# Kernel optimization log

Hardware: AMD Instinct MI355X
Metric: run time of the kernel (lower is better)

Reference implementation:

```python
import jax, jax.numpy as jnp
import numpy as np

N = 100000
E = 3200000
IN_DIM, HID_DIM, OUT_DIM = 29, 64, 2


def setup_inputs() -> dict:
    key = jax.random.key(0)
    k1, k2, k3, k4, k5 = jax.random.split(key, 5)
    x = jax.random.normal(k1, (N, IN_DIM), dtype=jnp.float32)
    edge_index = jax.random.randint(k2, (2, E), 0, N, dtype=jnp.int64)
    # GCNConv params: glorot-ish weights, zero bias (bias added after aggregation)
    W1 = jax.random.normal(k3, (IN_DIM, HID_DIM), dtype=jnp.float32) * (1.0 / np.sqrt(IN_DIM))
    b1 = jnp.zeros((HID_DIM,), dtype=jnp.float32)
    W2 = jax.random.normal(k4, (HID_DIM, OUT_DIM), dtype=jnp.float32) * (1.0 / np.sqrt(HID_DIM))
    b2 = jnp.zeros((OUT_DIM,), dtype=jnp.float32)
    return {"x": x, "edge_index": edge_index, "W1": W1, "b1": b1, "W2": W2, "b2": b2}


def _gcn_norm(edge_index, n_nodes):
    # PyG gcn_norm with add_self_loops=True, symmetric D^-1/2 A D^-1/2
    loop = jnp.arange(n_nodes, dtype=edge_index.dtype)
    src = jnp.concatenate([edge_index[0], loop])
    dst = jnp.concatenate([edge_index[1], loop])
    deg = jax.ops.segment_sum(jnp.ones_like(dst, dtype=jnp.float32), dst, num_segments=n_nodes)
    dinv = jnp.where(deg > 0, jax.lax.rsqrt(deg), 0.0)
    norm = dinv[src] * dinv[dst]  # [E + N]
    return src, dst, norm


def _gcn_conv(x, src, dst, norm, W, b):
    h = x @ W                      # [N, d_out] -- transform first (smaller msgs)
    msg = h[src] * norm[:, None]   # [E+N, d_out] gather + scale
    out = jax.ops.segment_sum(msg, dst, num_segments=x.shape[0])  # scatter-add
    return out + b


def reference(x, edge_index, W1, b1, W2, b2):
    src, dst, norm = _gcn_norm(edge_index, x.shape[0])
    h = _gcn_conv(x, src, dst, norm, W1, b1)
    h = jax.nn.relu(h)
    out = _gcn_conv(h, src, dst, norm, W2, b2)
    return out
```

## Files before the change

### kernel.cpp

```cpp
#include <hip/hip_runtime.h>

#define N_NODES 100000
#define N_EDGES 3200000
#define IN_DIM  29
#define HID_DIM 64
#define NBUCK   391
#define BNODES  256
#define CAP     10496
#define PEPT    16
#define PEPB    16384
#define PSTAGE  22272

#define OFF_CUR   0
#define OFF_ROWS  512
#define OFF_ROWE  100512
#define OFF_DINV  200512
#define OFF_ZS    300512
#define OFF_EBUF  500544
#define OFF_XS    4604480

static __device__ __forceinline__ unsigned short f2bf(float f) {
    unsigned u = __float_as_uint(f);
    u += 0x7fffu + ((u >> 16) & 1u);
    return (unsigned short)(u >> 16);
}

static __device__ __forceinline__ void unpack_add(float4& acc, uint2 a) {
    acc.x += __uint_as_float(a.x << 16);
    acc.y += __uint_as_float(a.x & 0xFFFF0000u);
    acc.z += __uint_as_float(a.y << 16);
    acc.w += __uint_as_float(a.y & 0xFFFF0000u);
}

__global__ __launch_bounds__(1024) void partition_kernel(const int* __restrict__ ei,
        int* __restrict__ gcursor, int* __restrict__ ebuf) {
    __shared__ int lhist[NBUCK];
    __shared__ int lcur[NBUCK];
    __shared__ int gbase[NBUCK];
    __shared__ int soff[NBUCK];
    __shared__ int sc[NBUCK];
    __shared__ int stage[PSTAGE];
    int tid = threadIdx.x;
    for (int i = tid; i < NBUCK; i += 1024) lhist[i] = 0;
    __syncthreads();

    int base = blockIdx.x * PEPB + tid * PEPT;
    bool valid = (base < N_EDGES);
    if (valid) {
        const int4* dp = (const int4*)(ei + N_EDGES + base);
        #pragma unroll
        for (int q = 0; q < 4; ++q) {
            int4 t = dp[q];
            atomicAdd(&lhist[t.x >> 8], 1); atomicAdd(&lhist[t.y >> 8], 1);
            atomicAdd(&lhist[t.z >> 8], 1); atomicAdd(&lhist[t.w >> 8], 1);
        }
    }
    __syncthreads();
    int c = 0, p = 0;
    if (tid < NBUCK) { c = lhist[tid]; p = (c + 15) & ~15; sc[tid] = p; }
    __syncthreads();
    for (int off = 1; off < NBUCK; off <<= 1) {
        int t = 0;
        if (tid < NBUCK && tid >= off) t = sc[tid - off];
        __syncthreads();
        if (tid < NBUCK) sc[tid] += t;
        __syncthreads();
    }
    if (tid < NBUCK) {
        int so = sc[tid] - p;
        soff[tid] = so;
        lcur[tid] = so;
        gbase[tid] = p ? (tid * CAP + atomicAdd(&gcursor[tid], p)) : 0;
    }
    __syncthreads();
    if (valid) {
        const int4* dp = (const int4*)(ei + N_EDGES + base);
        const int4* sp = (const int4*)(ei + base);
        #pragma unroll
        for (int q = 0; q < 4; ++q) {
            int4 d = dp[q];
            int4 s = sp[q];
            int pos;
            pos = atomicAdd(&lcur[d.x >> 8], 1); stage[pos] = s.x | ((d.x & 255) << 17);
            pos = atomicAdd(&lcur[d.y >> 8], 1); stage[pos] = s.y | ((d.y & 255) << 17);
            pos = atomicAdd(&lcur[d.z >> 8], 1); stage[pos] = s.z | ((d.z & 255) << 17);
            pos = atomicAdd(&lcur[d.w >> 8], 1); stage[pos] = s.w | ((d.w & 255) << 17);
        }
    }
    __syncthreads();
    if (tid < NBUCK) {
        int endReal = lcur[tid];
        int endPad  = soff[tid] + (((lhist[tid]) + 15) & ~15);
        for (int k = endReal; k < endPad; ++k) stage[k] = -1;
    }
    __syncthreads();
    int wv = tid >> 6, ln = tid & 63;
    for (int b = wv; b < NBUCK; b += 16) {
        int np = (lhist[b] + 15) & ~15;
        int so = soff[b], gb = gbase[b];
        for (int k = ln; k < np; k += 64)
            ebuf[gb + k] = stage[so + k];
    }
}

__global__ __launch_bounds__(1024) void bucketsort_kernel(const int* __restrict__ gcursor,
        int* __restrict__ ebuf, int* __restrict__ rowStart, int* __restrict__ rowEnd,
        float* __restrict__ dinv, const float* __restrict__ x,
        unsigned int* __restrict__ xsb, float* __restrict__ zs) {
    __shared__ int   cnt[BNODES];
    __shared__ int   cur[BNODES];
    __shared__ float dls[BNODES];
    __shared__ int   stage[CAP];
    __shared__ int   szp_sh;
    int b = blockIdx.x, tid = threadIdx.x;
    if (tid < BNODES) cnt[tid] = 0;
    __syncthreads();
    int base = b * CAP;
    int size = gcursor[b];

    for (int j = tid; j < size; j += 1024) {
        unsigned p = (unsigned)ebuf[base + j];
        if (p != 0xFFFFFFFFu) atomicAdd(&cnt[p >> 17], 1);
    }
    __syncthreads();

    int v = 0, vp = 0;
    if (tid < BNODES) { v = cnt[tid]; vp = (v + 7) & ~7; cur[tid] = vp; }
    __syncthreads();
    for (int off = 1; off < BNODES; off <<= 1) {
        int t = 0;
        if (tid < BNODES && tid >= off) t = cur[tid - off];
        __syncthreads();
        if (tid < BNODES) cur[tid] += t;
        __syncthreads();
    }
    if (tid < BNODES) {
        int excl = cur[tid] - vp;
        int node = b * BNODES + tid;
        if (node < N_NODES) {
            rowStart[node] = base + excl;
            rowEnd[node]   = base + excl + vp;
            float dn = rsqrtf((float)v + 1.0f);
            dinv[node] = dn;
            dls[tid] = dn;
        }
        if (tid == BNODES - 1) szp_sh = cur[tid];
        cur[tid] = excl;
        for (int p2 = excl + v; p2 < excl + vp; ++p2)
            stage[p2] = N_NODES;
    }
    __syncthreads();

    for (int j = tid; j < size; j += 1024) {
        unsigned p = (unsigned)ebuf[base + j];
        if (p != 0xFFFFFFFFu) {
            int pos = atomicAdd(&cur[p >> 17], 1);
            stage[pos] = p & 0x1FFFF;
        }
    }
    __syncthreads();
    int szp = szp_sh;
    for (int j = tid; j < szp; j += 1024)
        ebuf[base + j] = stage[j];

    for (int i = tid; i < BNODES * 16; i += 1024) {
        int dl = i >> 4, kp = i & 15;
        int nd = b * BNODES + dl;
        if (nd < N_NODES) {
            float dn = dls[dl];
            int k0 = kp * 2, k1 = k0 + 1;
            float f0 = (k0 < IN_DIM) ? x[nd * IN_DIM + k0] * dn : 0.0f;
            float f1 = (k1 < IN_DIM) ? x[nd * IN_DIM + k1] * dn : 0.0f;
            xsb[(size_t)nd * 16 + kp] = (unsigned)f2bf(f0) | ((unsigned)f2bf(f1) << 16);
        } else if (nd == N_NODES) {
            xsb[(size_t)nd * 16 + kp] = 0u;
        }
    }
    if (b == 0 && tid == 0) {
        zs[2 * N_NODES]     = 0.0f;
        zs[2 * N_NODES + 1] = 0.0f;
    }
}

#define XROW(i) (((unsigned)(i) << 6) | moff)

#define PREP(P, rs, re, node)                                            \
    int P##i0, P##i1, P##i2, P##i3, P##i4, P##i5;                        \
    {                                                                    \
        int relim = max((re) - 1, (rs));                                 \
        int j0 = (rs) + q;                                               \
        int t0 = ebuf[min(j0,      relim)];                              \
        int t1 = ebuf[min(j0 + 8,  relim)];                              \
        int t2 = ebuf[min(j0 + 16, relim)];                              \
        int t3 = ebuf[min(j0 + 24, relim)];                              \
        int t4 = ebuf[min(j0 + 32, relim)];                              \
        P##i0 = (j0      < (re)) ? t0 : N_NODES;                         \
        P##i1 = (j0 + 8  < (re)) ? t1 : N_NODES;                         \
        P##i2 = (j0 + 16 < (re)) ? t2 : N_NODES;                         \
        P##i3 = (j0 + 24 < (re)) ? t3 : N_NODES;                         \
        P##i4 = (j0 + 32 < (re)) ? t4 : N_NODES;                         \
        P##i5 = (q == 0) ? (node) : N_NODES;    \
    }

#define GATH(G, P)                                                       \
    uint2 G##0 = *(const uint2*)(xb + XROW(P##i0));                      \
    uint2 G##1 = *(const uint2*)(xb + XROW(P##i1));                      \
    uint2 G##2 = *(const uint2*)(xb + XROW(P##i2));                      \
    uint2 G##3 = *(const uint2*)(xb + XROW(P##i3));                      \
    uint2 G##4 = *(const uint2*)(xb + XROW(P##i4));                      \
    uint2 G##5 = *(const uint2*)(xb + XROW(P##i5));

#define UNP(acc, G)                                                      \
    unpack_add(acc, G##0); unpack_add(acc, G##1); unpack_add(acc, G##2); \
    unpack_add(acc, G##3); unpack_add(acc, G##4); unpack_add(acc, G##5);

#define TAIL(acc, rs, re)                                                \
    {                                                                    \
        int j = (rs) + q + 40;                                           \
        while (j < (re)) {                  \
            int s = ebuf[j];                                             \
            uint2 a = *(const uint2*)(xb + XROW(s));                     \
            unpack_add(acc, a);                                          \
            j += 8;                                                      \
        }                                                                \
    }

static __device__ __forceinline__ void mlp_store(float4 acc, int node, int lane,
        const float* w1s, const float* b1s, const float* w2s,
        const float* __restrict__ dinv, float* __restrict__ zs) {
    #pragma unroll
    for (int msk = 8; msk <= 32; msk <<= 1) {
        acc.x += __shfl_xor(acc.x, msk);
        acc.y += __shfl_xor(acc.y, msk);
        acc.z += __shfl_xor(acc.z, msk);
        acc.w += __shfl_xor(acc.w, msk);
    }
    float dn = dinv[node];
    acc.x *= dn; acc.y *= dn; acc.z *= dn; acc.w *= dn;

    float h = b1s[lane];
    #pragma unroll
    for (int kk = 0; kk < IN_DIM; ++kk) {
        float comp = ((kk & 3) == 0) ? acc.x : ((kk & 3) == 1) ? acc.y
                   : ((kk & 3) == 2) ? acc.z : acc.w;
        h = fmaf(__shfl(comp, kk >> 2), w1s[kk * HID_DIM + lane], h);
    }
    h = fmaxf(h, 0.0f);

    float z0 = h * w2s[lane * 2 + 0];
    float z1 = h * w2s[lane * 2 + 1];
    #pragma unroll
    for (int off = 32; off > 0; off >>= 1) {
        z0 += __shfl_down(z0, off);
        z1 += __shfl_down(z1, off);
    }
    if (lane == 0) {
        float2 o; o.x = z0 * dn; o.y = z1 * dn;
        *(float2*)(zs + node * 2) = o;
    }
}

__global__ __launch_bounds__(256) void fused_kernel(const unsigned int* __restrict__ xs_,
        const int* __restrict__ rowStart, const int* __restrict__ rowEnd,
        const int* __restrict__ ebuf, const float* __restrict__ dinv,
        const float* __restrict__ W1, const float* __restrict__ b1,
        const float* __restrict__ W2, float* __restrict__ zs) {
    __shared__ float w1s[IN_DIM * HID_DIM];
    __shared__ float b1s[HID_DIM];
    __shared__ float w2s[HID_DIM * 2];
    const int tid = threadIdx.x;
    for (int i = tid; i < IN_DIM * HID_DIM; i += 256) w1s[i] = W1[i];
    if (tid < HID_DIM) {
        b1s[tid] = b1[tid];
        w2s[tid * 2 + 0] = W2[tid * 2 + 0];
        w2s[tid * 2 + 1] = W2[tid * 2 + 1];
    }
    __syncthreads();

    const int lane = tid & 63;
    const int q = lane >> 3, m = lane & 7;
    const unsigned moff = (unsigned)(m << 3);
    const char* xb = (const char*)xs_;
    const int n0 = blockIdx.x * 16 + (tid >> 6) * 4;

    const int rs0 = rowStart[n0+0], re0 = rowEnd[n0+0];
    const int rs1 = rowStart[n0+1], re1 = rowEnd[n0+1];
    const int rs2 = rowStart[n0+2], re2 = rowEnd[n0+2];
    const int rs3 = rowStart[n0+3], re3 = rowEnd[n0+3];

    PREP(pa, rs0, re0, n0+0)
    GATH(ga, pa)
    PREP(pb, rs1, re1, n0+1)
    float4 acc0 = make_float4(0.f, 0.f, 0.f, 0.f);
    UNP(acc0, ga)
    TAIL(acc0, rs0, re0)
    GATH(gb, pb)
    PREP(pc, rs2, re2, n0+2)
    mlp_store(acc0, n0+0, lane, w1s, b1s, w2s, dinv, zs);

    float4 acc1 = make_float4(0.f, 0.f, 0.f, 0.f);
    UNP(acc1, gb)
    TAIL(acc1, rs1, re1)
    GATH(gc, pc)
    PREP(pd, rs3, re3, n0+3)
    mlp_store(acc1, n0+1, lane, w1s, b1s, w2s, dinv, zs);

    float4 acc2 = make_float4(0.f, 0.f, 0.f, 0.f);
    UNP(acc2, gc)
    TAIL(acc2, rs2, re2)
    GATH(gd, pd)
    mlp_store(acc2, n0+2, lane, w1s, b1s, w2s, dinv, zs);

    float4 acc3 = make_float4(0.f, 0.f, 0.f, 0.f);
    UNP(acc3, gd)
    TAIL(acc3, rs3, re3)
    mlp_store(acc3, n0+3, lane, w1s, b1s, w2s, dinv, zs);
}

__global__ __launch_bounds__(256) void agg2_kernel(const float* __restrict__ zs,
        const int* __restrict__ rowStart, const int* __restrict__ rowEnd,
        const int* __restrict__ ebuf, const float* __restrict__ dinv,
        const float* __restrict__ b2, float* __restrict__ out) {
    int tid = threadIdx.x;
    int node = blockIdx.x * 16 + (tid >> 4);
    if (node >= N_NODES) return;
    int gl = tid & 15;
    const float2* zs2 = (const float2*)zs;
    float a0 = 0.0f, a1 = 0.0f, c0 = 0.0f, c1 = 0.0f;
    int rs = rowStart[node], re = rowEnd[node];
    int j = rs + gl;
    for (; j + 16 < re; j += 32) {
        float2 za = zs2[ebuf[j]];
        float2 zb = zs2[ebuf[j + 16]];
        a0 += za.x; a1 += za.y;
        c0 += zb.x; c1 += zb.y;
    }
    if (j < re) {
        float2 za = zs2[ebuf[j]];
        a0 += za.x; a1 += za.y;
    }
    a0 += c0; a1 += c1;
    a0 += __shfl_xor(a0, 8); a1 += __shfl_xor(a1, 8);
    a0 += __shfl_xor(a0, 4); a1 += __shfl_xor(a1, 4);
    a0 += __shfl_xor(a0, 2); a1 += __shfl_xor(a1, 2);
    a0 += __shfl_xor(a0, 1); a1 += __shfl_xor(a1, 1);
    if (gl == 0) {
        float dn = dinv[node];
        float2 zself = zs2[node];
        float2 o;
        o.x = dn * (a0 + zself.x) + b2[0];
        o.y = dn * (a1 + zself.y) + b2[1];
        ((float2*)out)[node] = o;
    }
}

extern "C" void kernel_launch(void* const* d_in, const int* in_sizes, int n_in,
                              void* d_out, int out_size, void* d_ws, size_t ws_size,
                              hipStream_t stream) {
    const float* x  = (const float*)d_in[0];
    const int*   ei = (const int*)d_in[1];
    const float* W1 = (const float*)d_in[2];
    const float* b1 = (const float*)d_in[3];
    const float* W2 = (const float*)d_in[4];
    const float* b2 = (const float*)d_in[5];
    float* out = (float*)d_out;

    int*   wsi      = (int*)d_ws;
    float* wsf      = (float*)d_ws;
    int*   gcursor  = wsi + OFF_CUR;
    int*   rowStart = wsi + OFF_ROWS;
    int*   rowEnd   = wsi + OFF_ROWE;
    float* dinv     = wsf + OFF_DINV;
    float* zs       = wsf + OFF_ZS;
    int*   ebuf     = wsi + OFF_EBUF;
    unsigned int* xsb = (unsigned int*)(wsi + OFF_XS);

    hipMemsetAsync(gcursor, 0, NBUCK * sizeof(int), stream);
    partition_kernel<<<(N_EDGES + PEPB - 1) / PEPB, 1024, 0, stream>>>(ei, gcursor, ebuf);
    bucketsort_kernel<<<NBUCK, 1024, 0, stream>>>(gcursor, ebuf, rowStart, rowEnd, dinv, x, xsb, zs);
    fused_kernel<<<N_NODES / 16, 256, 0, stream>>>(xsb, rowStart, rowEnd, ebuf, dinv, W1, b1, W2, zs);
    agg2_kernel<<<(N_NODES + 15) / 16, 256, 0, stream>>>(zs, rowStart, rowEnd, ebuf, dinv, b2, out);
}
```

Before: 203.0 us.

## Split bf16 feature prep into its own kernel and pair MLP epilogues

Moves the scaled bf16 conversion of x out of bucketsort into a separate elementwise xs_kernel. Bucketsort now caches the raw partition entries in LDS and scatters sorted indices straight to global ebuf, dropping the LDS staging copy-back. The fused kernel moves to 512-thread blocks, issues more gathers earlier, and runs the MLP epilogue on two nodes at once so shuffles and FMAs can interleave. The cost is an extra kernel launch and scattered, uncoalesced global writes during the sort.

```diff
diff --git a/kernel.cpp b/kernel.cpp
--- a/kernel.cpp
+++ b/kernel.cpp
@@ -105,13 +105,10 @@
 
 __global__ __launch_bounds__(1024) void bucketsort_kernel(const int* __restrict__ gcursor,
         int* __restrict__ ebuf, int* __restrict__ rowStart, int* __restrict__ rowEnd,
-        float* __restrict__ dinv, const float* __restrict__ x,
-        unsigned int* __restrict__ xsb, float* __restrict__ zs) {
-    __shared__ int   cnt[BNODES];
-    __shared__ int   cur[BNODES];
-    __shared__ float dls[BNODES];
-    __shared__ int   stage[CAP];
-    __shared__ int   szp_sh;
+        float* __restrict__ dinv, float* __restrict__ zs) {
+    __shared__ int cnt[BNODES];
+    __shared__ int cur[BNODES];
+    __shared__ int stage[CAP];
     int b = blockIdx.x, tid = threadIdx.x;
     if (tid < BNODES) cnt[tid] = 0;
     __syncthreads();
@@ -120,6 +117,7 @@
 
     for (int j = tid; j < size; j += 1024) {
         unsigned p = (unsigned)ebuf[base + j];
+        stage[j] = (int)p;
         if (p != 0xFFFFFFFFu) atomicAdd(&cnt[p >> 17], 1);
     }
     __syncthreads();
@@ -140,46 +138,40 @@
         if (node < N_NODES) {
             rowStart[node] = base + excl;
             rowEnd[node]   = base + excl + vp;
-            float dn = rsqrtf((float)v + 1.0f);
-            dinv[node] = dn;
-            dls[tid] = dn;
+            dinv[node]     = rsqrtf((float)v + 1.0f);
+            for (int p2 = excl + v; p2 < excl + vp; ++p2)
+                ebuf[base + p2] = N_NODES;
         }
-        if (tid == BNODES - 1) szp_sh = cur[tid];
         cur[tid] = excl;
-        for (int p2 = excl + v; p2 < excl + vp; ++p2)
-            stage[p2] = N_NODES;
-    }
-    __syncthreads();
-
+    }
+    __syncthreads();
     for (int j = tid; j < size; j += 1024) {
-        unsigned p = (unsigned)ebuf[base + j];
+        unsigned p = (unsigned)stage[j];
         if (p != 0xFFFFFFFFu) {
             int pos = atomicAdd(&cur[p >> 17], 1);
-            stage[pos] = p & 0x1FFFF;
-        }
-    }
-    __syncthreads();
-    int szp = szp_sh;
-    for (int j = tid; j < szp; j += 1024)
-        ebuf[base + j] = stage[j];
-
-    for (int i = tid; i < BNODES * 16; i += 1024) {
-        int dl = i >> 4, kp = i & 15;
-        int nd = b * BNODES + dl;
-        if (nd < N_NODES) {
-            float dn = dls[dl];
-            int k0 = kp * 2, k1 = k0 + 1;
-            float f0 = (k0 < IN_DIM) ? x[nd * IN_DIM + k0] * dn : 0.0f;
-            float f1 = (k1 < IN_DIM) ? x[nd * IN_DIM + k1] * dn : 0.0f;
-            xsb[(size_t)nd * 16 + kp] = (unsigned)f2bf(f0) | ((unsigned)f2bf(f1) << 16);
-        } else if (nd == N_NODES) {
-            xsb[(size_t)nd * 16 + kp] = 0u;
+            ebuf[base + pos] = (int)(p & 0x1FFFF);
         }
     }
     if (b == 0 && tid == 0) {
         zs[2 * N_NODES]     = 0.0f;
         zs[2 * N_NODES + 1] = 0.0f;
     }
+}
+
+__global__ __launch_bounds__(256) void xs_kernel(const float* __restrict__ x,
+        const float* __restrict__ dinv, unsigned int* __restrict__ xsb) {
+    int i = blockIdx.x * 256 + threadIdx.x;
+    if (i >= (N_NODES + 1) * 16) return;
+    int nd = i >> 4, kp = i & 15;
+    unsigned u = 0u;
+    if (nd < N_NODES) {
+        float dn = dinv[nd];
+        int k0 = kp * 2, k1 = k0 + 1;
+        float f0 = (k0 < IN_DIM) ? x[nd * IN_DIM + k0] * dn : 0.0f;
+        float f1 = (k1 < IN_DIM) ? x[nd * IN_DIM + k1] * dn : 0.0f;
+        u = (unsigned)f2bf(f0) | ((unsigned)f2bf(f1) << 16);
+    }
+    xsb[i] = u;
 }
 
 #define XROW(i) (((unsigned)(i) << 6) | moff)
@@ -225,42 +217,50 @@
         }                                                                \
     }
 
-static __device__ __forceinline__ void mlp_store(float4 acc, int node, int lane,
+static __device__ __forceinline__ void mlp2_store(float4 aA, float4 aB,
+        int nodeA, int nodeB, int lane,
         const float* w1s, const float* b1s, const float* w2s,
         const float* __restrict__ dinv, float* __restrict__ zs) {
     #pragma unroll
     for (int msk = 8; msk <= 32; msk <<= 1) {
-        acc.x += __shfl_xor(acc.x, msk);
-        acc.y += __shfl_xor(acc.y, msk);
-        acc.z += __shfl_xor(acc.z, msk);
-        acc.w += __shfl_xor(acc.w, msk);
-    }
-    float dn = dinv[node];
-    acc.x *= dn; acc.y *= dn; acc.z *= dn; acc.w *= dn;
-
-    float h = b1s[lane];
+        aA.x += __shfl_xor(aA.x, msk); aB.x += __shfl_xor(aB.x, msk);
+        aA.y += __shfl_xor(aA.y, msk); aB.y += __shfl_xor(aB.y, msk);
+        aA.z += __shfl_xor(aA.z, msk); aB.z += __shfl_xor(aB.z, msk);
+        aA.w += __shfl_xor(aA.w, msk); aB.w += __shfl_xor(aB.w, msk);
+    }
+    float dnA = dinv[nodeA], dnB = dinv[nodeB];
+    aA.x *= dnA; aA.y *= dnA; aA.z *= dnA; aA.w *= dnA;
+    aB.x *= dnB; aB.y *= dnB; aB.z *= dnB; aB.w *= dnB;
+
+    float hA = b1s[lane], hB = b1s[lane];
     #pragma unroll
     for (int kk = 0; kk < IN_DIM; ++kk) {
-        float comp = ((kk & 3) == 0) ? acc.x : ((kk & 3) == 1) ? acc.y
-                   : ((kk & 3) == 2) ? acc.z : acc.w;
-        h = fmaf(__shfl(comp, kk >> 2), w1s[kk * HID_DIM + lane], h);
-    }
-    h = fmaxf(h, 0.0f);
-
-    float z0 = h * w2s[lane * 2 + 0];
-    float z1 = h * w2s[lane * 2 + 1];
+        float w = w1s[kk * HID_DIM + lane];
+        float cA = ((kk & 3) == 0) ? aA.x : ((kk & 3) == 1) ? aA.y
+                 : ((kk & 3) == 2) ? aA.z : aA.w;
+        float cB = ((kk & 3) == 0) ? aB.x : ((kk & 3) == 1) ? aB.y
+                 : ((kk & 3) == 2) ? aB.z : aB.w;
+        hA = fmaf(__shfl(cA, kk >> 2), w, hA);
+        hB = fmaf(__shfl(cB, kk >> 2), w, hB);
+    }
+    hA = fmaxf(hA, 0.0f); hB = fmaxf(hB, 0.0f);
+
+    float zA0 = hA * w2s[lane * 2 + 0], zA1 = hA * w2s[lane * 2 + 1];
+    float zB0 = hB * w2s[lane * 2 + 0], zB1 = hB * w2s[lane * 2 + 1];
     #pragma unroll
     for (int off = 32; off > 0; off >>= 1) {
-        z0 += __shfl_down(z0, off);
-        z1 += __shfl_down(z1, off);
+        zA0 += __shfl_down(zA0, off); zA1 += __shfl_down(zA1, off);
+        zB0 += __shfl_down(zB0, off); zB1 += __shfl_down(zB1, off);
     }
     if (lane == 0) {
-        float2 o; o.x = z0 * dn; o.y = z1 * dn;
-        *(float2*)(zs + node * 2) = o;
-    }
-}
-
-__global__ __launch_bounds__(256) void fused_kernel(const unsigned int* __restrict__ xs_,
+        float2 oA; oA.x = zA0 * dnA; oA.y = zA1 * dnA;
+        float2 oB; oB.x = zB0 * dnB; oB.y = zB1 * dnB;
+        *(float2*)(zs + nodeA * 2) = oA;
+        *(float2*)(zs + nodeB * 2) = oB;
+    }
+}
+
+__global__ __launch_bounds__(512) void fused_kernel(const unsigned int* __restrict__ xs_,
         const int* __restrict__ rowStart, const int* __restrict__ rowEnd,
         const int* __restrict__ ebuf, const float* __restrict__ dinv,
         const float* __restrict__ W1, const float* __restrict__ b1,
@@ -269,7 +269,7 @@
     __shared__ float b1s[HID_DIM];
     __shared__ float w2s[HID_DIM * 2];
     const int tid = threadIdx.x;
-    for (int i = tid; i < IN_DIM * HID_DIM; i += 256) w1s[i] = W1[i];
+    for (int i = tid; i < IN_DIM * HID_DIM; i += 512) w1s[i] = W1[i];
     if (tid < HID_DIM) {
         b1s[tid] = b1[tid];
         w2s[tid * 2 + 0] = W2[tid * 2 + 0];
@@ -281,7 +281,7 @@
     const int q = lane >> 3, m = lane & 7;
     const unsigned moff = (unsigned)(m << 3);
     const char* xb = (const char*)xs_;
-    const int n0 = blockIdx.x * 16 + (tid >> 6) * 4;
+    const int n0 = blockIdx.x * 32 + (tid >> 6) * 4;
 
     const int rs0 = rowStart[n0+0], re0 = rowEnd[n0+0];
     const int rs1 = rowStart[n0+1], re1 = rowEnd[n0+1];
@@ -289,32 +289,28 @@
     const int rs3 = rowStart[n0+3], re3 = rowEnd[n0+3];
 
     PREP(pa, rs0, re0, n0+0)
+    PREP(pb, rs1, re1, n0+1)
     GATH(ga, pa)
-    PREP(pb, rs1, re1, n0+1)
+    GATH(gb, pb)
+    PREP(pc, rs2, re2, n0+2)
+    PREP(pd, rs3, re3, n0+3)
     float4 acc0 = make_float4(0.f, 0.f, 0.f, 0.f);
+    float4 acc1 = make_float4(0.f, 0.f, 0.f, 0.f);
     UNP(acc0, ga)
     TAIL(acc0, rs0, re0)
-    GATH(gb, pb)
-    PREP(pc, rs2, re2, n0+2)
-    mlp_store(acc0, n0+0, lane, w1s, b1s, w2s, dinv, zs);
-
-    float4 acc1 = make_float4(0.f, 0.f, 0.f, 0.f);
     UNP(acc1, gb)
     TAIL(acc1, rs1, re1)
     GATH(gc, pc)
-    PREP(pd, rs3, re3, n0+3)
-    mlp_store(acc1, n0+1, lane, w1s, b1s, w2s, dinv, zs);
+    GATH(gd, pd)
+    mlp2_store(acc0, acc1, n0+0, n0+1, lane, w1s, b1s, w2s, dinv, zs);
 
     float4 acc2 = make_float4(0.f, 0.f, 0.f, 0.f);
+    float4 acc3 = make_float4(0.f, 0.f, 0.f, 0.f);
     UNP(acc2, gc)
     TAIL(acc2, rs2, re2)
-    GATH(gd, pd)
-    mlp_store(acc2, n0+2, lane, w1s, b1s, w2s, dinv, zs);
-
-    float4 acc3 = make_float4(0.f, 0.f, 0.f, 0.f);
     UNP(acc3, gd)
     TAIL(acc3, rs3, re3)
-    mlp_store(acc3, n0+3, lane, w1s, b1s, w2s, dinv, zs);
+    mlp2_store(acc2, acc3, n0+2, n0+3, lane, w1s, b1s, w2s, dinv, zs);
 }
 
 __global__ __launch_bounds__(256) void agg2_kernel(const float* __restrict__ zs,
@@ -377,7 +373,8 @@
 
     hipMemsetAsync(gcursor, 0, NBUCK * sizeof(int), stream);
     partition_kernel<<<(N_EDGES + PEPB - 1) / PEPB, 1024, 0, stream>>>(ei, gcursor, ebuf);
-    bucketsort_kernel<<<NBUCK, 1024, 0, stream>>>(gcursor, ebuf, rowStart, rowEnd, dinv, x, xsb, zs);
-    fused_kernel<<<N_NODES / 16, 256, 0, stream>>>(xsb, rowStart, rowEnd, ebuf, dinv, W1, b1, W2, zs);
+    bucketsort_kernel<<<NBUCK, 1024, 0, stream>>>(gcursor, ebuf, rowStart, rowEnd, dinv, zs);
+    xs_kernel<<<((N_NODES + 1) * 16 + 255) / 256, 256, 0, stream>>>(x, dinv, xsb);
+    fused_kernel<<<N_NODES / 32, 512, 0, stream>>>(xsb, rowStart, rowEnd, ebuf, dinv, W1, b1, W2, zs);
     agg2_kernel<<<(N_NODES + 15) / 16, 256, 0, stream>>>(zs, rowStart, rowEnd, ebuf, dinv, b2, out);
 }
```

Result: slower. 216.2 us (+6.5%).
